# Optimization experiments

Measured on AMD Instinct MI355X. Metric: run time of the kernel, lower is better.

The kernel has to match this reference:

```python
import jax, jax.numpy as jnp
from jax import lax
import numpy as np

B, L, H, O, T = 2048, 64, 128, 64, 512

def setup_inputs() -> dict:
    key = jax.random.key(0)
    ks = jax.random.split(key, 9)
    s = 0.05
    return {
        "latent": jax.random.normal(ks[0], (B, L), jnp.float32),
        "fc_w": jax.random.normal(ks[1], (H, L), jnp.float32) * s,
        "fc_b": jax.random.normal(ks[2], (H,), jnp.float32) * s,
        "W_ih": jax.random.normal(ks[3], (4 * H, H), jnp.float32) * s,
        "W_hh": jax.random.normal(ks[4], (4 * H, H), jnp.float32) * s,
        "b_ih": jax.random.normal(ks[5], (4 * H,), jnp.float32) * s,
        "b_hh": jax.random.normal(ks[6], (4 * H,), jnp.float32) * s,
        "Wo": jax.random.normal(ks[7], (O, H), jnp.float32) * s,
        "bo": jax.random.normal(ks[8], (O,), jnp.float32) * s,
        "seq_len": T,
    }

def reference(latent, fc_w, fc_b, W_ih, W_hh, b_ih, b_hh, Wo, bo, seq_len):
    # initial hidden from fc(latent); cell and first input are zeros
    h0 = latent @ fc_w.T + fc_b            # [B, H]
    c0 = jnp.zeros_like(h0)
    x0 = jnp.zeros_like(h0)

    def step(carry, _):
        x, h, c = carry
        gates = x @ W_ih.T + b_ih + h @ W_hh.T + b_hh   # [B, 4H]
        i, f, g, o = jnp.split(gates, 4, axis=-1)        # PyTorch gate order
        c = jax.nn.sigmoid(f) * c + jax.nn.sigmoid(i) * jnp.tanh(g)
        h = jax.nn.sigmoid(o) * jnp.tanh(c)
        out = h @ Wo.T + bo                              # [B, O]
        # the module feeds the LSTM output back as next input
        return (h, h, c), out

    _, outs = lax.scan(step, (x0, h0, c0), None, length=seq_len)
    return jnp.transpose(outs, (1, 0, 2))  # [B, T, O]
```

## Files before the change

kernel.cpp:

```cpp
#include <hip/hip_runtime.h>
#include <hip/hip_bf16.h>


#define H_DIM 128
#define L_DIM 64
#define O_DIM 64
#define ROWS 8
#define THREADS 512
#define LOG2E 1.44269504f

typedef __attribute__((ext_vector_type(4))) float f32x4;
typedef __attribute__((ext_vector_type(4))) float float4v;
typedef __attribute__((ext_vector_type(8))) __bf16 bf16x8;
typedef __attribute__((ext_vector_type(8))) unsigned short u16x8;

__device__ __forceinline__ float fast_exp2(float x) {
#if __has_builtin(__builtin_amdgcn_exp2f)
  return __builtin_amdgcn_exp2f(x);
#else
  return exp2f(x);
#endif
}
__device__ __forceinline__ float fast_rcp(float x) {
#if __has_builtin(__builtin_amdgcn_rcpf)
  return __builtin_amdgcn_rcpf(x);
#else
  return 1.0f / x;
#endif
}
__device__ __forceinline__ float sigm_y(float y) {
  return fast_rcp(1.0f + fast_exp2(-y));
}
__device__ __forceinline__ float tanh_y(float y) {
  return 1.0f - 2.0f * fast_rcp(1.0f + fast_exp2(y));
}
__device__ __forceinline__ unsigned short f2bf(float f) {
  unsigned u; __builtin_memcpy(&u, &f, 4);
  u = (u + 0x7FFFu + ((u >> 16) & 1u)) >> 16;
  return (unsigned short)u;
}
__device__ __forceinline__ void split2(float v, unsigned short& hi, unsigned short& lo) {
  __bf16 hb = (__bf16)v;
  __bf16 lb = (__bf16)(v - (float)hb);
  hi = __builtin_bit_cast(unsigned short, hb);
  lo = __builtin_bit_cast(unsigned short, lb);
}

__device__ __forceinline__ void load_wfrags(const float* __restrict__ W_ih,
                                            const float* __restrict__ W_hh,
                                            bool add_ih, int ub, int k0,
                                            bf16x8 wf[4][4]) {
  const float gsc[4] = {LOG2E, LOG2E, 2.0f * LOG2E, LOG2E};
#pragma unroll
  for (int g = 0; g < 4; ++g) {
    const float* ph = W_hh + (size_t)(g * 128 + ub) * H_DIM + k0;
    const float* pi = W_ih + (size_t)(g * 128 + ub) * H_DIM + k0;
    const float s = gsc[g];
#pragma unroll
    for (int kk = 0; kk < 4; ++kk) {
      float4v x0 = *(const float4v*)(ph + kk * 32);
      float4v x1 = *(const float4v*)(ph + kk * 32 + 4);
      if (add_ih) {
        x0 += *(const float4v*)(pi + kk * 32);
        x1 += *(const float4v*)(pi + kk * 32 + 4);
      }
      u16x8 b;
#pragma unroll
      for (int e = 0; e < 4; ++e) {
        b[e] = f2bf(s * x0[e]);
        b[e + 4] = f2bf(s * x1[e]);
      }
      wf[g][kk] = __builtin_bit_cast(bf16x8, b);
    }
  }
}

__global__ __launch_bounds__(THREADS, 2) void lstm_decoder_kernel(
    const float* __restrict__ latent, const float* __restrict__ fc_w,
    const float* __restrict__ fc_b, const float* __restrict__ W_ih,
    const float* __restrict__ W_hh, const float* __restrict__ b_ih,
    const float* __restrict__ b_hh, const float* __restrict__ Wo,
    const float* __restrict__ bo, const int* __restrict__ seq_len_p,
    float* __restrict__ out) {
  const int tid = threadIdx.x;
  const int lane = tid & 63;
  const int w = tid >> 6;
  const int row0 = blockIdx.x * ROWS;
  const int T = seq_len_p[0];

  __shared__ __align__(16) unsigned short hbuf[2][16 * 128];

  {
    const int u = tid & 127;
    const int rbase = tid >> 7;
#pragma unroll
    for (int pp = 0; pp < 2; ++pp) {
      const int bl = rbase + pp * 4;
      const float4v* lat4 = (const float4v*)(latent + (size_t)(row0 + bl) * L_DIM);
      const float4v* fw4  = (const float4v*)(fc_w + (size_t)u * L_DIM);
      float s = fc_b[u];
#pragma unroll
      for (int j = 0; j < L_DIM / 4; ++j) {
        float4v a = lat4[j], b = fw4[j];
        s += a[0] * b[0] + a[1] * b[1] + a[2] * b[2] + a[3] * b[3];
      }
      const int mh = 2 * bl, ml = 2 * bl + 1;
      unsigned short hh, ll;
      split2(s, hh, ll);
      *(unsigned short*)((char*)hbuf[0] + ((unsigned)(mh * 256 + u * 2) ^ ((mh & 7) << 4))) = hh;
      *(unsigned short*)((char*)hbuf[0] + ((unsigned)(ml * 256 + u * 2) ^ ((ml & 7) << 4))) = ll;
    }
  }

  const int ub = (w << 4) + (lane & 15);
  const int k0 = (lane >> 4) << 3;
  const float gscb[4] = {LOG2E, LOG2E, 2.0f * LOG2E, LOG2E};
  float bias_g[4];
#pragma unroll
  for (int g = 0; g < 4; ++g)
    bias_g[g] = gscb[g] * (b_ih[g * 128 + ub] + b_hh[g * 128 + ub]);

  const int ocol = ((w & 3) << 4) + (lane & 15);
  const float bo_l = bo[ocol];

  bf16x8 wofrag[4];
#pragma unroll
  for (int kk = 0; kk < 4; ++kk) {
    const float* p = Wo + (size_t)ocol * H_DIM + k0 + kk * 32;
    float4v x0 = *(const float4v*)p;
    float4v x1 = *(const float4v*)(p + 4);
    u16x8 b;
#pragma unroll
    for (int e = 0; e < 4; ++e) { b[e] = f2bf(x0[e]); b[e + 4] = f2bf(x1[e]); }
    wofrag[kk] = __builtin_bit_cast(bf16x8, b);
  }

  bf16x8 wf[4][4];
  load_wfrags(W_ih, W_hh, false, ub, k0, wf);

  __syncthreads();

  bf16x8 af[4];
  const unsigned asw = (unsigned)(((lane & 15) & 7) << 4);
  const unsigned abase = (unsigned)((lane & 15) * 256 + ((lane >> 4) << 4));
#pragma unroll
  for (int kk = 0; kk < 4; ++kk)
    af[kk] = *(const bf16x8*)((const char*)hbuf[0] + ((abase + kk * 64) ^ asw));

  const int lg = lane >> 4;
  unsigned woff[4];
#pragma unroll
  for (int r = 0; r < 4; ++r) {
    const int m = 4 * lg + r;
    woff[r] = (unsigned)((m * 256 + ub * 2) ^ ((m & 7) << 4));
  }

  float cA = 0.0f, cB = 0.0f;
  float* pa = out + (size_t)(row0 + 2 * lg) * T * O_DIM + ocol;
  float* pb = out + (size_t)(row0 + 2 * lg + 1) * T * O_DIM + ocol;

  auto halfstep = [&](unsigned short* __restrict__ dst, bool reload) {
    f32x4 acc[4];
#pragma unroll
    for (int g = 0; g < 4; ++g) {
      f32x4 a = {bias_g[g], 0.0f, bias_g[g], 0.0f};
#pragma unroll
      for (int kk = 0; kk < 4; ++kk)
        a = __builtin_amdgcn_mfma_f32_16x16x32_bf16(af[kk], wf[g][kk], a, 0, 0, 0);
      acc[g] = a;
    }

    float hA, hB;
    {
      float yi = acc[0][0] + acc[0][1], yf = acc[1][0] + acc[1][1];
      float yg = acc[2][0] + acc[2][1], yo = acc[3][0] + acc[3][1];
      cA = sigm_y(yf) * cA + sigm_y(yi) * tanh_y(yg);
      hA = sigm_y(yo) * tanh_y(2.0f * LOG2E * cA);
      yi = acc[0][2] + acc[0][3]; yf = acc[1][2] + acc[1][3];
      yg = acc[2][2] + acc[2][3]; yo = acc[3][2] + acc[3][3];
      cB = sigm_y(yf) * cB + sigm_y(yi) * tanh_y(yg);
      hB = sigm_y(yo) * tanh_y(2.0f * LOG2E * cB);
    }

    {
      unsigned short hh, ll;
      split2(hA, hh, ll);
      *(unsigned short*)((char*)dst + woff[0]) = hh;
      *(unsigned short*)((char*)dst + woff[1]) = ll;
      split2(hB, hh, ll);
      *(unsigned short*)((char*)dst + woff[2]) = hh;
      *(unsigned short*)((char*)dst + woff[3]) = ll;
    }

    if (reload)
      load_wfrags(W_ih, W_hh, true, ub, k0, wf);

    __syncthreads();

#pragma unroll
    for (int kk = 0; kk < 4; ++kk)
      af[kk] = *(const bf16x8*)((const char*)dst + ((abase + kk * 64) ^ asw));

    if (w < 4) {
      f32x4 ao = {bo_l, 0.0f, bo_l, 0.0f};
#pragma unroll
      for (int kk = 0; kk < 4; ++kk)
        ao = __builtin_amdgcn_mfma_f32_16x16x32_bf16(af[kk], wofrag[kk], ao, 0, 0, 0);
      *pa = ao[0] + ao[1];
      *pb = ao[2] + ao[3];
    }
    pa += O_DIM;
    pb += O_DIM;
  };

#pragma unroll 1
  for (int tt = 0; tt < (T >> 1); ++tt) {
    halfstep(hbuf[1], tt == 0);
    halfstep(hbuf[0], false);
  }
  if (T & 1) halfstep(hbuf[1], T == 1);
}

extern "C" void kernel_launch(void* const* d_in, const int* in_sizes, int n_in,
                              void* d_out, int out_size, void* d_ws, size_t ws_size,
                              hipStream_t stream) {
  const float* latent = (const float*)d_in[0];
  const float* fc_w   = (const float*)d_in[1];
  const float* fc_b   = (const float*)d_in[2];
  const float* W_ih   = (const float*)d_in[3];
  const float* W_hh   = (const float*)d_in[4];
  const float* b_ih   = (const float*)d_in[5];
  const float* b_hh   = (const float*)d_in[6];
  const float* Wo     = (const float*)d_in[7];
  const float* bo     = (const float*)d_in[8];
  const int* seq_len  = (const int*)d_in[9];
  float* out = (float*)d_out;

  const int B = in_sizes[0] / L_DIM;
  const int blocks = B / ROWS;

  hipLaunchKernelGGL(lstm_decoder_kernel, dim3(blocks), dim3(THREADS), 0, stream,
                     latent, fc_w, fc_b, W_ih, W_hh, b_ih, b_hh, Wo, bo, seq_len, out);
}
```

Measured before the change: 340.4 us.

## Overlap output projection with gate MFMAs and widen LDS swizzle

The output projection for the previous step's hidden state now runs right after the gate MFMAs, using the same A fragments, instead of after the barrier. Its result is stored in the next half-step, with a tail projection after the loop for the last step. This takes the output MFMA chain and store off the serial path between barrier and next step. The LDS XOR swizzle also folds in bit 3 of the row index to cut bank conflicts, at the cost of extra registers and slightly more complex control flow.

Measured after the change: 347.5 us. +2.1%, slower.

```diff
diff --git a/kernel.cpp b/kernel.cpp
--- a/kernel.cpp
+++ b/kernel.cpp
@@ -14,6 +14,9 @@
 typedef __attribute__((ext_vector_type(8))) __bf16 bf16x8;
 typedef __attribute__((ext_vector_type(8))) unsigned short u16x8;
 
+__device__ __forceinline__ unsigned swzf(int r) {
+  return (unsigned)(((r & 7) << 4) ^ ((r & 8) << 2));
+}
 __device__ __forceinline__ float fast_exp2(float x) {
 #if __has_builtin(__builtin_amdgcn_exp2f)
   return __builtin_amdgcn_exp2f(x);
@@ -107,8 +110,8 @@
       const int mh = 2 * bl, ml = 2 * bl + 1;
       unsigned short hh, ll;
       split2(s, hh, ll);
-      *(unsigned short*)((char*)hbuf[0] + ((unsigned)(mh * 256 + u * 2) ^ ((mh & 7) << 4))) = hh;
-      *(unsigned short*)((char*)hbuf[0] + ((unsigned)(ml * 256 + u * 2) ^ ((ml & 7) << 4))) = ll;
+      *(unsigned short*)((char*)hbuf[0] + ((unsigned)(mh * 256 + u * 2) ^ swzf(mh))) = hh;
+      *(unsigned short*)((char*)hbuf[0] + ((unsigned)(ml * 256 + u * 2) ^ swzf(ml))) = ll;
     }
   }
 
@@ -141,7 +144,7 @@
   __syncthreads();
 
   bf16x8 af[4];
-  const unsigned asw = (unsigned)(((lane & 15) & 7) << 4);
+  const unsigned asw = swzf(lane & 15);
   const unsigned abase = (unsigned)((lane & 15) * 256 + ((lane >> 4) << 4));
 #pragma unroll
   for (int kk = 0; kk < 4; ++kk)
@@ -152,14 +155,14 @@
 #pragma unroll
   for (int r = 0; r < 4; ++r) {
     const int m = 4 * lg + r;
-    woff[r] = (unsigned)((m * 256 + ub * 2) ^ ((m & 7) << 4));
+    woff[r] = (unsigned)((m * 256 + ub * 2) ^ swzf(m));
   }
 
   float cA = 0.0f, cB = 0.0f;
   float* pa = out + (size_t)(row0 + 2 * lg) * T * O_DIM + ocol;
   float* pb = out + (size_t)(row0 + 2 * lg + 1) * T * O_DIM + ocol;
 
-  auto halfstep = [&](unsigned short* __restrict__ dst, bool reload) {
+  auto halfstep = [&](unsigned short* dst, bool first, bool reload) {
     f32x4 acc[4];
 #pragma unroll
     for (int g = 0; g < 4; ++g) {
@@ -168,6 +171,15 @@
       for (int kk = 0; kk < 4; ++kk)
         a = __builtin_amdgcn_mfma_f32_16x16x32_bf16(af[kk], wf[g][kk], a, 0, 0, 0);
       acc[g] = a;
+    }
+
+    f32x4 ao = {0.0f, 0.0f, 0.0f, 0.0f};
+    if (w < 4) {
+      f32x4 a = {bo_l, 0.0f, bo_l, 0.0f};
+#pragma unroll
+      for (int kk = 0; kk < 4; ++kk)
+        a = __builtin_amdgcn_mfma_f32_16x16x32_bf16(af[kk], wofrag[kk], a, 0, 0, 0);
+      ao = a;
     }
 
     float hA, hB;
@@ -197,28 +209,33 @@
 
     __syncthreads();
 
+    if (w < 4 && !first) {
+      *pa = ao[0] + ao[1];
+      *pb = ao[2] + ao[3];
+      pa += O_DIM;
+      pb += O_DIM;
+    }
+
 #pragma unroll
     for (int kk = 0; kk < 4; ++kk)
       af[kk] = *(const bf16x8*)((const char*)dst + ((abase + kk * 64) ^ asw));
-
-    if (w < 4) {
-      f32x4 ao = {bo_l, 0.0f, bo_l, 0.0f};
-#pragma unroll
-      for (int kk = 0; kk < 4; ++kk)
-        ao = __builtin_amdgcn_mfma_f32_16x16x32_bf16(af[kk], wofrag[kk], ao, 0, 0, 0);
-      *pa = ao[0] + ao[1];
-      *pb = ao[2] + ao[3];
-    }
-    pa += O_DIM;
-    pb += O_DIM;
   };
 
 #pragma unroll 1
   for (int tt = 0; tt < (T >> 1); ++tt) {
-    halfstep(hbuf[1], tt == 0);
-    halfstep(hbuf[0], false);
-  }
-  if (T & 1) halfstep(hbuf[1], T == 1);
+    halfstep(hbuf[1], tt == 0, tt == 0);
+    halfstep(hbuf[0], false, false);
+  }
+  if (T & 1) halfstep(hbuf[1], T == 1, T == 1);
+
+  if (w < 4 && T > 0) {
+    f32x4 a = {bo_l, 0.0f, bo_l, 0.0f};
+#pragma unroll
+    for (int kk = 0; kk < 4; ++kk)
+      a = __builtin_amdgcn_mfma_f32_16x16x32_bf16(af[kk], wofrag[kk], a, 0, 0, 0);
+    *pa = a[0] + a[1];
+    *pb = a[2] + a[3];
+  }
 }
 
 extern "C" void kernel_launch(void* const* d_in, const int* in_sizes, int n_in,
```

## Share reciprocals across paired LSTM gates, add MFMA priority, widen LDS swizzle

Applied to the files above, without the earlier changes.

Gate nonlinearities for the two rows each thread owns now share reciprocals: the two denominators are multiplied together, one rcp is taken, and each result is recovered by multiplying back, which cuts transcendental rcp calls per step. The sigmoid(i)*tanh(g) product is fused into a single rational expression. s_setprio is raised around the MFMA blocks to favour matrix issue across waves, and the LDS XOR swizzle now also mixes row bit 3 to reduce bank conflicts. Multiplying denominators risks overflow to inf for large gate magnitudes, which could produce NaN or zero where the original stayed finite.

New measurement: 325.0 us. -4.5%, faster.

```diff
diff --git a/kernel.cpp b/kernel.cpp
--- a/kernel.cpp
+++ b/kernel.cpp
@@ -14,6 +14,9 @@
 typedef __attribute__((ext_vector_type(8))) __bf16 bf16x8;
 typedef __attribute__((ext_vector_type(8))) unsigned short u16x8;
 
+__device__ __forceinline__ unsigned swzf(int r) {
+  return (unsigned)(((r & 7) << 4) ^ ((r & 8) << 2));
+}
 __device__ __forceinline__ float fast_exp2(float x) {
 #if __has_builtin(__builtin_amdgcn_exp2f)
   return __builtin_amdgcn_exp2f(x);
@@ -27,12 +30,6 @@
 #else
   return 1.0f / x;
 #endif
-}
-__device__ __forceinline__ float sigm_y(float y) {
-  return fast_rcp(1.0f + fast_exp2(-y));
-}
-__device__ __forceinline__ float tanh_y(float y) {
-  return 1.0f - 2.0f * fast_rcp(1.0f + fast_exp2(y));
 }
 __device__ __forceinline__ unsigned short f2bf(float f) {
   unsigned u; __builtin_memcpy(&u, &f, 4);
@@ -107,8 +104,8 @@
       const int mh = 2 * bl, ml = 2 * bl + 1;
       unsigned short hh, ll;
       split2(s, hh, ll);
-      *(unsigned short*)((char*)hbuf[0] + ((unsigned)(mh * 256 + u * 2) ^ ((mh & 7) << 4))) = hh;
-      *(unsigned short*)((char*)hbuf[0] + ((unsigned)(ml * 256 + u * 2) ^ ((ml & 7) << 4))) = ll;
+      *(unsigned short*)((char*)hbuf[0] + ((unsigned)(mh * 256 + u * 2) ^ swzf(mh))) = hh;
+      *(unsigned short*)((char*)hbuf[0] + ((unsigned)(ml * 256 + u * 2) ^ swzf(ml))) = ll;
     }
   }
 
@@ -141,7 +138,7 @@
   __syncthreads();
 
   bf16x8 af[4];
-  const unsigned asw = (unsigned)(((lane & 15) & 7) << 4);
+  const unsigned asw = swzf(lane & 15);
   const unsigned abase = (unsigned)((lane & 15) * 256 + ((lane >> 4) << 4));
 #pragma unroll
   for (int kk = 0; kk < 4; ++kk)
@@ -152,15 +149,16 @@
 #pragma unroll
   for (int r = 0; r < 4; ++r) {
     const int m = 4 * lg + r;
-    woff[r] = (unsigned)((m * 256 + ub * 2) ^ ((m & 7) << 4));
+    woff[r] = (unsigned)((m * 256 + ub * 2) ^ swzf(m));
   }
 
   float cA = 0.0f, cB = 0.0f;
   float* pa = out + (size_t)(row0 + 2 * lg) * T * O_DIM + ocol;
   float* pb = out + (size_t)(row0 + 2 * lg + 1) * T * O_DIM + ocol;
 
-  auto halfstep = [&](unsigned short* __restrict__ dst, bool reload) {
+  auto halfstep = [&](unsigned short* dst, bool reload) {
     f32x4 acc[4];
+    __builtin_amdgcn_s_setprio(1);
 #pragma unroll
     for (int g = 0; g < 4; ++g) {
       f32x4 a = {bias_g[g], 0.0f, bias_g[g], 0.0f};
@@ -169,17 +167,40 @@
         a = __builtin_amdgcn_mfma_f32_16x16x32_bf16(af[kk], wf[g][kk], a, 0, 0, 0);
       acc[g] = a;
     }
+    __builtin_amdgcn_s_setprio(0);
 
     float hA, hB;
     {
-      float yi = acc[0][0] + acc[0][1], yf = acc[1][0] + acc[1][1];
-      float yg = acc[2][0] + acc[2][1], yo = acc[3][0] + acc[3][1];
-      cA = sigm_y(yf) * cA + sigm_y(yi) * tanh_y(yg);
-      hA = sigm_y(yo) * tanh_y(2.0f * LOG2E * cA);
-      yi = acc[0][2] + acc[0][3]; yf = acc[1][2] + acc[1][3];
-      yg = acc[2][2] + acc[2][3]; yo = acc[3][2] + acc[3][3];
-      cB = sigm_y(yf) * cB + sigm_y(yi) * tanh_y(yg);
-      hB = sigm_y(yo) * tanh_y(2.0f * LOG2E * cB);
+      float yiA = acc[0][0] + acc[0][1], yfA = acc[1][0] + acc[1][1];
+      float ygA = acc[2][0] + acc[2][1], yoA = acc[3][0] + acc[3][1];
+      float yiB = acc[0][2] + acc[0][3], yfB = acc[1][2] + acc[1][3];
+      float ygB = acc[2][2] + acc[2][3], yoB = acc[3][2] + acc[3][3];
+
+      float EiA = fast_exp2(-yiA), EfA = fast_exp2(-yfA);
+      float GgA = fast_exp2(ygA),  EoA = fast_exp2(-yoA);
+      float EiB = fast_exp2(-yiB), EfB = fast_exp2(-yfB);
+      float GgB = fast_exp2(ygB),  EoB = fast_exp2(-yoB);
+
+      float DfA = 1.0f + EfA, DfB = 1.0f + EfB;
+      float rf = fast_rcp(DfA * DfB);
+      float sfA = rf * DfB, sfB = rf * DfA;
+
+      float DiGA = (1.0f + EiA) * (1.0f + GgA);
+      float DiGB = (1.0f + EiB) * (1.0f + GgB);
+      float rg = fast_rcp(DiGA * DiGB);
+      float sitA = (GgA - 1.0f) * (rg * DiGB);
+      float sitB = (GgB - 1.0f) * (rg * DiGA);
+
+      cA = sfA * cA + sitA;
+      cB = sfB * cB + sitB;
+
+      float tcA = 1.0f - 2.0f * fast_rcp(1.0f + fast_exp2(2.0f * LOG2E * cA));
+      float tcB = 1.0f - 2.0f * fast_rcp(1.0f + fast_exp2(2.0f * LOG2E * cB));
+
+      float DoA = 1.0f + EoA, DoB = 1.0f + EoB;
+      float ro = fast_rcp(DoA * DoB);
+      hA = (ro * DoB) * tcA;
+      hB = (ro * DoA) * tcB;
     }
 
     {
@@ -203,9 +224,11 @@
 
     if (w < 4) {
       f32x4 ao = {bo_l, 0.0f, bo_l, 0.0f};
+      __builtin_amdgcn_s_setprio(1);
 #pragma unroll
       for (int kk = 0; kk < 4; ++kk)
         ao = __builtin_amdgcn_mfma_f32_16x16x32_bf16(af[kk], wofrag[kk], ao, 0, 0, 0);
+      __builtin_amdgcn_s_setprio(0);
       *pa = ao[0] + ao[1];
       *pb = ao[2] + ao[3];
     }
```

## Switch recurrent and output matmuls from split-bf16 to int8 MFMA with row scaling

Applied to the files above, without the earlier changes.

Quantizes the recurrent and output weights to int8 with per-row scales, and encodes the hidden state as a hi/lo int8 pair instead of a hi/lo bf16 pair. The per-step GEMMs then use 16x16x64 i8 MFMA, which halves the MFMA count and the LDS traffic. The gate nonlinearities are restructured to share reciprocals across the two rows, and MFMA sections are raised in wave priority. This adds quantization error: the weights carry only about 7 bits of precision and the initial hidden state is clamped, so accuracy over a 512-step recurrence is at risk.

New measurement: 412.9 us. 21.3% more time.

```diff
diff --git a/kernel.cpp b/kernel.cpp
--- a/kernel.cpp
+++ b/kernel.cpp
@@ -9,11 +9,12 @@
 #define THREADS 512
 #define LOG2E 1.44269504f
 
-typedef __attribute__((ext_vector_type(4))) float f32x4;
 typedef __attribute__((ext_vector_type(4))) float float4v;
-typedef __attribute__((ext_vector_type(8))) __bf16 bf16x8;
-typedef __attribute__((ext_vector_type(8))) unsigned short u16x8;
-
+typedef __attribute__((ext_vector_type(4))) int i32x4;
+
+__device__ __forceinline__ unsigned swzf(int r) {
+  return (unsigned)(((r & 7) << 4) ^ ((r & 8) << 2));
+}
 __device__ __forceinline__ float fast_exp2(float x) {
 #if __has_builtin(__builtin_amdgcn_exp2f)
   return __builtin_amdgcn_exp2f(x);
@@ -28,51 +29,75 @@
   return 1.0f / x;
 #endif
 }
-__device__ __forceinline__ float sigm_y(float y) {
-  return fast_rcp(1.0f + fast_exp2(-y));
-}
-__device__ __forceinline__ float tanh_y(float y) {
-  return 1.0f - 2.0f * fast_rcp(1.0f + fast_exp2(y));
-}
-__device__ __forceinline__ unsigned short f2bf(float f) {
-  unsigned u; __builtin_memcpy(&u, &f, 4);
-  u = (u + 0x7FFFu + ((u >> 16) & 1u)) >> 16;
-  return (unsigned short)u;
-}
-__device__ __forceinline__ void split2(float v, unsigned short& hi, unsigned short& lo) {
-  __bf16 hb = (__bf16)v;
-  __bf16 lb = (__bf16)(v - (float)hb);
-  hi = __builtin_bit_cast(unsigned short, hb);
-  lo = __builtin_bit_cast(unsigned short, lb);
-}
-
-__device__ __forceinline__ void load_wfrags(const float* __restrict__ W_ih,
-                                            const float* __restrict__ W_hh,
-                                            bool add_ih, int ub, int k0,
-                                            bf16x8 wf[4][4]) {
-  const float gsc[4] = {LOG2E, LOG2E, 2.0f * LOG2E, LOG2E};
-#pragma unroll
-  for (int g = 0; g < 4; ++g) {
-    const float* ph = W_hh + (size_t)(g * 128 + ub) * H_DIM + k0;
-    const float* pi = W_ih + (size_t)(g * 128 + ub) * H_DIM + k0;
-    const float s = gsc[g];
-#pragma unroll
-    for (int kk = 0; kk < 4; ++kk) {
-      float4v x0 = *(const float4v*)(ph + kk * 32);
-      float4v x1 = *(const float4v*)(ph + kk * 32 + 4);
-      if (add_ih) {
-        x0 += *(const float4v*)(pi + kk * 32);
-        x1 += *(const float4v*)(pi + kk * 32 + 4);
+
+__device__ __forceinline__ void quant_row1(const float* __restrict__ ph,
+                                           const float* __restrict__ pi,
+                                           bool add_ih, float gs, int k0,
+                                           i32x4 wq[2], float& kc) {
+  float mx = 1e-20f;
+#pragma unroll
+  for (int j = 0; j < 32; ++j) {
+    float4v x = *(const float4v*)(ph + 4 * j);
+    if (add_ih) x += *(const float4v*)(pi + 4 * j);
+#pragma unroll
+    for (int e = 0; e < 4; ++e) mx = fmaxf(mx, __builtin_fabsf(x[e]));
+  }
+  mx *= gs;
+  const float inv = 127.0f * fast_rcp(mx);
+#pragma unroll
+  for (int half = 0; half < 2; ++half) {
+    unsigned wd[4];
+#pragma unroll
+    for (int d = 0; d < 4; ++d) {
+      unsigned accw = 0;
+#pragma unroll
+      for (int e = 0; e < 4; ++e) {
+        const int k = half * 64 + k0 + d * 4 + e;
+        float v = ph[k];
+        if (add_ih) v += pi[k];
+        float q = __builtin_rintf(v * gs * inv);
+        q = fminf(fmaxf(q, -127.0f), 127.0f);
+        accw |= ((unsigned)((int)q & 255)) << (8 * e);
       }
-      u16x8 b;
+      wd[d] = accw;
+    }
+    wq[half] = (i32x4){(int)wd[0], (int)wd[1], (int)wd[2], (int)wd[3]};
+  }
+  kc = mx * (1.0f / (127.0f * 16256.0f));
+}
+
+__device__ __forceinline__ void quant_row2(const float* __restrict__ p, int k0,
+                                           i32x4 qh[2], i32x4 ql[2], float& kc) {
+  float mx = 1e-20f;
+#pragma unroll
+  for (int j = 0; j < 32; ++j) {
+    float4v x = *(const float4v*)(p + 4 * j);
+#pragma unroll
+    for (int e = 0; e < 4; ++e) mx = fmaxf(mx, __builtin_fabsf(x[e]));
+  }
+  const float inv = 127.0f * fast_rcp(mx);
+#pragma unroll
+  for (int half = 0; half < 2; ++half) {
+    unsigned wh[4], wl[4];
+#pragma unroll
+    for (int d = 0; d < 4; ++d) {
+      unsigned ah = 0, al = 0;
 #pragma unroll
       for (int e = 0; e < 4; ++e) {
-        b[e] = f2bf(s * x0[e]);
-        b[e + 4] = f2bf(s * x1[e]);
+        const int k = half * 64 + k0 + d * 4 + e;
+        float u = p[k] * inv;
+        float qhf = __builtin_rintf(u);
+        qhf = fminf(fmaxf(qhf, -127.0f), 127.0f);
+        float qlf = __builtin_rintf((u - qhf) * 128.0f);
+        ah |= ((unsigned)((int)qhf & 255)) << (8 * e);
+        al |= ((unsigned)((int)qlf & 255)) << (8 * e);
       }
-      wf[g][kk] = __builtin_bit_cast(bf16x8, b);
-    }
-  }
+      wh[d] = ah; wl[d] = al;
+    }
+    qh[half] = (i32x4){(int)wh[0], (int)wh[1], (int)wh[2], (int)wh[3]};
+    ql[half] = (i32x4){(int)wl[0], (int)wl[1], (int)wl[2], (int)wl[3]};
+  }
+  kc = mx * (1.0f / (127.0f * 16256.0f));
 }
 
 __global__ __launch_bounds__(THREADS, 2) void lstm_decoder_kernel(
@@ -88,7 +113,7 @@
   const int row0 = blockIdx.x * ROWS;
   const int T = seq_len_p[0];
 
-  __shared__ __align__(16) unsigned short hbuf[2][16 * 128];
+  __shared__ __align__(16) signed char hbuf[2][16 * 128];
 
   {
     const int u = tid & 127;
@@ -104,110 +129,148 @@
         float4v a = lat4[j], b = fw4[j];
         s += a[0] * b[0] + a[1] * b[1] + a[2] * b[2] + a[3] * b[3];
       }
+      s = fminf(fmaxf(s, -3.99f), 3.99f);
+      float qhf = __builtin_rintf(s * 31.75f);
+      int hi8 = (int)qhf;
+      float r = fmaf(qhf, -4.0f / 127.0f, s);
+      int lo8 = (int)__builtin_rintf(r * 4064.0f);
       const int mh = 2 * bl, ml = 2 * bl + 1;
-      unsigned short hh, ll;
-      split2(s, hh, ll);
-      *(unsigned short*)((char*)hbuf[0] + ((unsigned)(mh * 256 + u * 2) ^ ((mh & 7) << 4))) = hh;
-      *(unsigned short*)((char*)hbuf[0] + ((unsigned)(ml * 256 + u * 2) ^ ((ml & 7) << 4))) = ll;
+      hbuf[0][(unsigned)(mh * 128 + u) ^ swzf(mh)] = (signed char)hi8;
+      hbuf[0][(unsigned)(ml * 128 + u) ^ swzf(ml)] = (signed char)lo8;
     }
   }
 
   const int ub = (w << 4) + (lane & 15);
-  const int k0 = (lane >> 4) << 3;
+  const int k0 = (lane >> 4) << 4;
   const float gscb[4] = {LOG2E, LOG2E, 2.0f * LOG2E, LOG2E};
-  float bias_g[4];
+  float bias_y[4];
 #pragma unroll
   for (int g = 0; g < 4; ++g)
-    bias_g[g] = gscb[g] * (b_ih[g * 128 + ub] + b_hh[g * 128 + ub]);
+    bias_y[g] = gscb[g] * (b_ih[g * 128 + ub] + b_hh[g * 128 + ub]);
 
   const int ocol = ((w & 3) << 4) + (lane & 15);
   const float bo_l = bo[ocol];
 
-  bf16x8 wofrag[4];
-#pragma unroll
-  for (int kk = 0; kk < 4; ++kk) {
-    const float* p = Wo + (size_t)ocol * H_DIM + k0 + kk * 32;
-    float4v x0 = *(const float4v*)p;
-    float4v x1 = *(const float4v*)(p + 4);
-    u16x8 b;
-#pragma unroll
-    for (int e = 0; e < 4; ++e) { b[e] = f2bf(x0[e]); b[e + 4] = f2bf(x1[e]); }
-    wofrag[kk] = __builtin_bit_cast(bf16x8, b);
-  }
-
-  bf16x8 wf[4][4];
-  load_wfrags(W_ih, W_hh, false, ub, k0, wf);
+  i32x4 woh[2], wol[2];
+  float kO;
+  quant_row2(Wo + (size_t)ocol * H_DIM, k0, woh, wol, kO);
+
+  i32x4 wfq[4][2];
+  float kc[4];
+#pragma unroll
+  for (int g = 0; g < 4; ++g)
+    quant_row1(W_hh + (size_t)(g * 128 + ub) * H_DIM,
+               W_ih + (size_t)(g * 128 + ub) * H_DIM,
+               false, gscb[g], k0, wfq[g], kc[g]);
 
   __syncthreads();
 
-  bf16x8 af[4];
-  const unsigned asw = (unsigned)(((lane & 15) & 7) << 4);
-  const unsigned abase = (unsigned)((lane & 15) * 256 + ((lane >> 4) << 4));
-#pragma unroll
-  for (int kk = 0; kk < 4; ++kk)
-    af[kk] = *(const bf16x8*)((const char*)hbuf[0] + ((abase + kk * 64) ^ asw));
+  const int arow = lane & 15;
+  const unsigned aoff0 = (unsigned)(arow * 128 + k0) ^ swzf(arow);
+  const unsigned aoff1 = (unsigned)(arow * 128 + 64 + k0) ^ swzf(arow);
+  i32x4 af[2];
+  af[0] = *(const i32x4*)((const signed char*)hbuf[0] + aoff0);
+  af[1] = *(const i32x4*)((const signed char*)hbuf[0] + aoff1);
 
   const int lg = lane >> 4;
   unsigned woff[4];
 #pragma unroll
   for (int r = 0; r < 4; ++r) {
     const int m = 4 * lg + r;
-    woff[r] = (unsigned)((m * 256 + ub * 2) ^ ((m & 7) << 4));
+    woff[r] = (unsigned)(m * 128 + ub) ^ swzf(m);
   }
 
   float cA = 0.0f, cB = 0.0f;
   float* pa = out + (size_t)(row0 + 2 * lg) * T * O_DIM + ocol;
   float* pb = out + (size_t)(row0 + 2 * lg + 1) * T * O_DIM + ocol;
 
-  auto halfstep = [&](unsigned short* __restrict__ dst, bool reload) {
-    f32x4 acc[4];
+  auto halfstep = [&](signed char* dst, bool reload, float ascale) {
+    i32x4 acc[4];
+    __builtin_amdgcn_s_setprio(1);
 #pragma unroll
     for (int g = 0; g < 4; ++g) {
-      f32x4 a = {bias_g[g], 0.0f, bias_g[g], 0.0f};
-#pragma unroll
-      for (int kk = 0; kk < 4; ++kk)
-        a = __builtin_amdgcn_mfma_f32_16x16x32_bf16(af[kk], wf[g][kk], a, 0, 0, 0);
+      i32x4 a = {0, 0, 0, 0};
+      a = __builtin_amdgcn_mfma_i32_16x16x64_i8(af[0], wfq[g][0], a, 0, 0, 0);
+      a = __builtin_amdgcn_mfma_i32_16x16x64_i8(af[1], wfq[g][1], a, 0, 0, 0);
       acc[g] = a;
+    }
+    __builtin_amdgcn_s_setprio(0);
+
+    float yv[8];
+#pragma unroll
+    for (int g = 0; g < 4; ++g) {
+      const float kg = kc[g] * ascale;
+      const int giA = acc[g][0] * 128 + acc[g][1];
+      const int giB = acc[g][2] * 128 + acc[g][3];
+      yv[g]     = fmaf((float)giA, kg, bias_y[g]);
+      yv[4 + g] = fmaf((float)giB, kg, bias_y[g]);
     }
 
     float hA, hB;
     {
-      float yi = acc[0][0] + acc[0][1], yf = acc[1][0] + acc[1][1];
-      float yg = acc[2][0] + acc[2][1], yo = acc[3][0] + acc[3][1];
-      cA = sigm_y(yf) * cA + sigm_y(yi) * tanh_y(yg);
-      hA = sigm_y(yo) * tanh_y(2.0f * LOG2E * cA);
-      yi = acc[0][2] + acc[0][3]; yf = acc[1][2] + acc[1][3];
-      yg = acc[2][2] + acc[2][3]; yo = acc[3][2] + acc[3][3];
-      cB = sigm_y(yf) * cB + sigm_y(yi) * tanh_y(yg);
-      hB = sigm_y(yo) * tanh_y(2.0f * LOG2E * cB);
+      float EfA = fast_exp2(-yv[1]), EfB = fast_exp2(-yv[5]);
+      float DfA = 1.0f + EfA, DfB = 1.0f + EfB;
+      float rf = fast_rcp(DfA * DfB);
+      float sfA = rf * DfB, sfB = rf * DfA;
+
+      float EiA = fast_exp2(-yv[0]), GA = fast_exp2(yv[2]);
+      float EiB = fast_exp2(-yv[4]), GB = fast_exp2(yv[6]);
+      float DgA = (1.0f + EiA) * (1.0f + GA);
+      float DgB = (1.0f + EiB) * (1.0f + GB);
+      float rg = fast_rcp(DgA * DgB);
+      float sitA = (GA - 1.0f) * (rg * DgB);
+      float sitB = (GB - 1.0f) * (rg * DgA);
+
+      cA = fmaf(sfA, cA, sitA);
+      cB = fmaf(sfB, cB, sitB);
+      cA = fminf(fmaxf(cA, -15.0f), 15.0f);
+      cB = fminf(fmaxf(cB, -15.0f), 15.0f);
+
+      float CA = fast_exp2(2.0f * LOG2E * cA), EoA = fast_exp2(-yv[3]);
+      float CB = fast_exp2(2.0f * LOG2E * cB), EoB = fast_exp2(-yv[7]);
+      float PoA = (1.0f + EoA) * (1.0f + CA);
+      float PoB = (1.0f + EoB) * (1.0f + CB);
+      float rc = fast_rcp(PoA * PoB);
+      hA = (CA - 1.0f) * (rc * PoB);
+      hB = (CB - 1.0f) * (rc * PoA);
     }
 
     {
-      unsigned short hh, ll;
-      split2(hA, hh, ll);
-      *(unsigned short*)((char*)dst + woff[0]) = hh;
-      *(unsigned short*)((char*)dst + woff[1]) = ll;
-      split2(hB, hh, ll);
-      *(unsigned short*)((char*)dst + woff[2]) = hh;
-      *(unsigned short*)((char*)dst + woff[3]) = ll;
-    }
-
-    if (reload)
-      load_wfrags(W_ih, W_hh, true, ub, k0, wf);
+      float qhf = __builtin_rintf(hA * 127.0f);
+      float r = fmaf(qhf, -1.0f / 127.0f, hA);
+      dst[woff[0]] = (signed char)(int)qhf;
+      dst[woff[1]] = (signed char)(int)__builtin_rintf(r * 16256.0f);
+      qhf = __builtin_rintf(hB * 127.0f);
+      r = fmaf(qhf, -1.0f / 127.0f, hB);
+      dst[woff[2]] = (signed char)(int)qhf;
+      dst[woff[3]] = (signed char)(int)__builtin_rintf(r * 16256.0f);
+    }
+
+    if (reload) {
+#pragma unroll
+      for (int g = 0; g < 4; ++g)
+        quant_row1(W_hh + (size_t)(g * 128 + ub) * H_DIM,
+                   W_ih + (size_t)(g * 128 + ub) * H_DIM,
+                   true, gscb[g], k0, wfq[g], kc[g]);
+    }
 
     __syncthreads();
 
-#pragma unroll
-    for (int kk = 0; kk < 4; ++kk)
-      af[kk] = *(const bf16x8*)((const char*)dst + ((abase + kk * 64) ^ asw));
+    af[0] = *(const i32x4*)((const signed char*)dst + aoff0);
+    af[1] = *(const i32x4*)((const signed char*)dst + aoff1);
 
     if (w < 4) {
-      f32x4 ao = {bo_l, 0.0f, bo_l, 0.0f};
-#pragma unroll
-      for (int kk = 0; kk < 4; ++kk)
-        ao = __builtin_amdgcn_mfma_f32_16x16x32_bf16(af[kk], wofrag[kk], ao, 0, 0, 0);
-      *pa = ao[0] + ao[1];
-      *pb = ao[2] + ao[3];
+      i32x4 p1 = {0, 0, 0, 0}, p2 = {0, 0, 0, 0};
+      __builtin_amdgcn_s_setprio(1);
+      p1 = __builtin_amdgcn_mfma_i32_16x16x64_i8(af[0], woh[0], p1, 0, 0, 0);
+      p1 = __builtin_amdgcn_mfma_i32_16x16x64_i8(af[1], woh[1], p1, 0, 0, 0);
+      p2 = __builtin_amdgcn_mfma_i32_16x16x64_i8(af[0], wol[0], p2, 0, 0, 0);
+      p2 = __builtin_amdgcn_mfma_i32_16x16x64_i8(af[1], wol[1], p2, 0, 0, 0);
+      __builtin_amdgcn_s_setprio(0);
+      const int oiA = (p1[0] * 128 + p1[1]) + p2[0] + (p2[1] >> 7);
+      const int oiB = (p1[2] * 128 + p1[3]) + p2[2] + (p2[3] >> 7);
+      *pa = fmaf((float)oiA, kO, bo_l);
+      *pb = fmaf((float)oiB, kO, bo_l);
     }
     pa += O_DIM;
     pb += O_DIM;
@@ -215,10 +278,10 @@
 
 #pragma unroll 1
   for (int tt = 0; tt < (T >> 1); ++tt) {
-    halfstep(hbuf[1], tt == 0);
-    halfstep(hbuf[0], false);
-  }
-  if (T & 1) halfstep(hbuf[1], T == 1);
+    halfstep(hbuf[1], tt == 0, tt == 0 ? 4.0f : 1.0f);
+    halfstep(hbuf[0], false, 1.0f);
+  }
+  if (T & 1) halfstep(hbuf[1], T == 1, T == 1 ? 4.0f : 1.0f);
 }
 
 extern "C" void kernel_launch(void* const* d_in, const int* in_sizes, int n_in,
```
